# Kernel tuning notes

Measured on AMD Instinct MI355X. Metric: run time of the kernel, lower is better.

The kernel has to match this reference:

```python
import jax, jax.numpy as jnp
import numpy as np
import math

B, N, DIM, H, DH = 4, 1024, 512, 8, 64
INNER = H * DH
TEMP = 0.1
REG_LAMBDA = 0.3
LARGE_NEG = -1.0e9


def setup_inputs() -> dict:
    key = jax.random.key(0)
    ks = jax.random.split(key, 10)
    x = jax.random.normal(ks[0], (B, N, DIM), dtype=jnp.float32)
    # binary channel mask with guaranteed self-connection on the diagonal
    m = jax.random.randint(ks[1], (B, N, N), 0, 2, dtype=jnp.int32)
    eye_i = jnp.eye(N, dtype=jnp.int32)[None]
    attn_mask = jnp.maximum(m, eye_i)
    s = 0.02
    Wq = jax.random.normal(ks[2], (DIM, INNER), dtype=jnp.float32) * s
    bq = jnp.zeros((INNER,), dtype=jnp.float32)
    Wk = jax.random.normal(ks[3], (DIM, INNER), dtype=jnp.float32) * s
    bk = jnp.zeros((INNER,), dtype=jnp.float32)
    Wv = jax.random.normal(ks[4], (DIM, INNER), dtype=jnp.float32) * s
    bv = jnp.zeros((INNER,), dtype=jnp.float32)
    Wo = jax.random.normal(ks[5], (INNER, DIM), dtype=jnpp_dummy()) * s if False else jax.random.normal(ks[5], (INNER, DIM), dtype=jnp.float32) * s
    bo = jnp.zeros((DIM,), dtype=jnp.float32)
    return {"x": x, "attn_mask": attn_mask, "Wq": Wq, "bq": bq, "Wk": Wk,
            "bk": bk, "Wv": Wv, "bv": bv, "Wo": Wo, "bo": bo}


def jnp_dummy():
    return jnp.float32


def _split_heads(t):
    # [b, n, h*d] -> [b, h, n, d]
    return t.reshape(t.shape[0], t.shape[1], H, DH).transpose(0, 2, 1, 3)


def _dynamical_contrastive_loss(scores, attn_mask_f, norm_matrix):
    # cosine similarity matrix (scores / |q||k|)
    cos = scores / norm_matrix
    e = jnp.exp(cos / TEMP)                                   # [b,h,n,n]
    pos = (e * attn_mask_f[:, None]).sum(-1)                  # [b,h,n]
    allsum = e.sum(-1)                                        # [b,h,n]
    clustering = -jnp.log(pos / allsum)
    eye = jnp.eye(N, dtype=attn_mask_f.dtype)
    regular = jnp.abs(attn_mask_f - eye[None]).sum((-2, -1)) / (N * (N - 1))
    return clustering.mean() + REG_LAMBDA * regular.mean()


def reference(x, attn_mask, Wq, bq, Wk, bk, Wv, bv, Wo, bo):
    q = _split_heads(x @ Wq + bq)  # [b,h,n,d]
    k = _split_heads(x @ Wk + bk)
    v = _split_heads(x @ Wv + bv)
    scale = 1.0 / math.sqrt(DH)

    scores = jnp.einsum('bhid,bhjd->bhij', q, k)
    q_norm = jnp.linalg.norm(q, axis=-1, keepdims=True)       # [b,h,n,1]
    k_norm = jnp.linalg.norm(k, axis=-1, keepdims=True)
    norm_matrix = q_norm * jnp.swapaxes(k_norm, -1, -2)       # [b,h,n,n]

    am = attn_mask.astype(scores.dtype)[:, None]              # [b,1,n,n]
    masked_scores = scores * am + (1.0 - am) * LARGE_NEG
    # faithful replication of the all-blocked-row special case
    # (-1e9 is finite so this is a no-op unless scores contain -inf)
    row_all_blocked = jnp.all(jnp.isneginf(masked_scores), axis=-1, keepdims=True)
    masked_scores = jnp.where(row_all_blocked, jnp.zeros_like(masked_scores), masked_scores)

    dcl = _dynamical_contrastive_loss(scores, attn_mask.astype(scores.dtype), norm_matrix)

    attn = jax.nn.softmax(masked_scores * scale, axis=-1)
    out = jnp.einsum('bhij,bhjd->bhid', attn, v)
    out = out.transpose(0, 2, 1, 3).reshape(x.shape[0], x.shape[1], INNER)
    # dropout is identity in eval mode
    return out @ Wo + bo, attn, dcl
```

## Files before the change

### kernel.cpp

```cpp
#include <hip/hip_runtime.h>
#include <hip/hip_bf16.h>
#include <math.h>

#define BB 4
#define NTOK 1024
#define DIMD 512
#define HH 8
#define DH 64
#define INNER 512
#define BH (BB*HH)
#define ROWS (BB*NTOK)
#define SCALE 0.125f
#define INV_TEMP 10.0f

typedef __bf16 bf16_t;
using bf16x4 = __attribute__((ext_vector_type(4))) __bf16;
using bf16x8 = __attribute__((ext_vector_type(8))) __bf16;
using f32x4  = __attribute__((ext_vector_type(4))) float;

__device__ __forceinline__ int swz(int row, int e) { return e ^ ((row & 7) << 3); }

template<int TM, int TN, int MT, int NT>
__device__ __forceinline__ void gemm_core(
    const bf16_t* __restrict__ A, int ldA,
    const bf16_t* __restrict__ B, int ldB, int K,
    bf16_t* As, bf16_t* Bs, f32x4 (&acc)[MT][NT])
{
    const int t = threadIdx.x;
    const int w = t >> 6, l = t & 63;
    constexpr int WGN = TN / (NT * 16);
    const int wm = w / WGN, wn = w % WGN;
    const int lrow = l & 15, lk = (l >> 4) * 8;

    for (int k0 = 0; k0 < K; k0 += 32) {
        #pragma unroll
        for (int it = 0; it < TM / 64; ++it) {
            int r = (t >> 2) + it * 64;
            *(uint4*)&As[r * 32 + (t & 3) * 8] =
                *(const uint4*)&A[(size_t)r * ldA + k0 + (t & 3) * 8];
        }
        #pragma unroll
        for (int it = 0; it < TN / 64; ++it) {
            int r = (t >> 2) + it * 64;
            *(uint4*)&Bs[r * 32 + (t & 3) * 8] =
                *(const uint4*)&B[(size_t)r * ldB + k0 + (t & 3) * 8];
        }
        __syncthreads();
        bf16x8 af[MT], bf[NT];
        #pragma unroll
        for (int mt = 0; mt < MT; ++mt)
            af[mt] = *(const bf16x8*)&As[(wm * MT * 16 + mt * 16 + lrow) * 32 + lk];
        #pragma unroll
        for (int nt = 0; nt < NT; ++nt)
            bf[nt] = *(const bf16x8*)&Bs[(wn * NT * 16 + nt * 16 + lrow) * 32 + lk];
        #pragma unroll
        for (int mt = 0; mt < MT; ++mt)
            #pragma unroll
            for (int nt = 0; nt < NT; ++nt)
                acc[mt][nt] = __builtin_amdgcn_mfma_f32_16x16x32_bf16(
                    af[mt], bf[nt], acc[mt][nt], 0, 0, 0);
        __syncthreads();
    }
}

__global__ __launch_bounds__(256) void convert_x(
    const float* __restrict__ x, bf16_t* __restrict__ xb)
{
    int idx = blockIdx.x * 256 + threadIdx.x;
    float4 v = ((const float4*)x)[idx];
    bf16x4 o = { (bf16_t)v.x, (bf16_t)v.y, (bf16_t)v.z, (bf16_t)v.w };
    ((bf16x4*)xb)[idx] = o;
}

__global__ __launch_bounds__(256) void mask_pack(
    const int* __restrict__ mask, unsigned int* __restrict__ mp)
{
    const int rr = blockIdx.x, b = blockIdx.y, c = threadIdx.x;
    const int* mb = mask + ((size_t)(b * NTOK + rr * 4)) * NTOK;
    #pragma unroll
    for (int u = 0; u < 4; ++u) {
        int col = u * 256 + c;
        unsigned int o = (unsigned)mb[col]
                       | ((unsigned)mb[NTOK + col] << 8)
                       | ((unsigned)mb[2 * NTOK + col] << 16)
                       | ((unsigned)mb[3 * NTOK + col] << 24);
        mp[((size_t)b * 256 + rr) * NTOK + col] = o;
    }
}

__global__ __launch_bounds__(256) void transpose_w(
    const float* __restrict__ Wq, const float* __restrict__ Wk,
    const float* __restrict__ Wv, const float* __restrict__ Wo,
    bf16_t* __restrict__ wt)
{
    __shared__ float tile[32][33];
    const int z = blockIdx.z;
    const float* src = (z == 0) ? Wq : (z == 1) ? Wk : (z == 2) ? Wv : Wo;
    bf16_t* dst = wt + (size_t)z * DIMD * INNER;
    const int t = threadIdx.x, tx = t & 31, ty = t >> 5;
    const int rBase = blockIdx.y * 32, cBase = blockIdx.x * 32;
    #pragma unroll
    for (int i = 0; i < 4; ++i)
        tile[ty + i * 8][tx] = src[(size_t)(rBase + ty + i * 8) * INNER + cBase + tx];
    __syncthreads();
    #pragma unroll
    for (int i = 0; i < 4; ++i)
        dst[(size_t)(cBase + ty + i * 8) * DIMD + rBase + tx] = (bf16_t)tile[tx][ty + i * 8];
}

__global__ __launch_bounds__(256) void qkv_gemm(
    const bf16_t* __restrict__ xb, const bf16_t* __restrict__ wt,
    const float* __restrict__ bq, const float* __restrict__ bk,
    const float* __restrict__ bv,
    bf16_t* __restrict__ qb, bf16_t* __restrict__ kb, bf16_t* __restrict__ vt)
{
    __shared__ __align__(16) bf16_t As[128 * 32];
    __shared__ __align__(16) bf16_t Bs[128 * 32];
    const int z = blockIdx.z;
    const bf16_t* Bp = wt + (size_t)z * DIMD * INNER;
    const float* bias = (z == 0) ? bq : (z == 1) ? bk : bv;
    const int rowBase = blockIdx.y * 128, colBase = blockIdx.x * 128;

    f32x4 acc[4][4] = {};
    gemm_core<128, 128, 4, 4>(xb + (size_t)rowBase * DIMD, DIMD,
                              Bp + (size_t)colBase * DIMD, DIMD, DIMD,
                              As, Bs, acc);

    const int l = threadIdx.x & 63, w = threadIdx.x >> 6;
    const int wm = w >> 1, wn = w & 1;
    #pragma unroll
    for (int mt = 0; mt < 4; ++mt)
        #pragma unroll
        for (int nt = 0; nt < 4; ++nt)
            #pragma unroll
            for (int r = 0; r < 4; ++r) {
                int grow = rowBase + wm * 64 + mt * 16 + (l >> 4) * 4 + r;
                int gcol = colBase + wn * 64 + nt * 16 + (l & 15);
                float val = acc[mt][nt][r] + bias[gcol];
                int b = grow >> 10, n = grow & 1023, h = gcol >> 6, d = gcol & 63;
                if (z == 0)
                    qb[(((size_t)b * HH + h) * NTOK + n) * DH + d] = (bf16_t)val;
                else if (z == 1)
                    kb[(((size_t)b * HH + h) * NTOK + n) * DH + d] = (bf16_t)val;
                else
                    vt[(((size_t)b * HH + h) * DH + d) * NTOK + n] = (bf16_t)val;
            }
}

__global__ __launch_bounds__(256) void norm_kernel(
    const bf16_t* __restrict__ qb, const bf16_t* __restrict__ kb,
    float* __restrict__ iqn, float* __restrict__ ikn)
{
    const int row = blockIdx.x * 4 + (threadIdx.x >> 6);
    const int d = threadIdx.x & 63;
    const bf16_t* src = blockIdx.y ? kb : qb;
    float* dst = blockIdx.y ? ikn : iqn;
    float v = (float)src[(size_t)row * DH + d];
    float s = v * v;
    #pragma unroll
    for (int off = 32; off; off >>= 1) s += __shfl_down(s, off);
    if (d == 0) dst[row] = 1.0f / sqrtf(s);
}

__global__ __launch_bounds__(256) void stats_gemm(
    const bf16_t* __restrict__ qb, const bf16_t* __restrict__ kb,
    const unsigned int* __restrict__ mp,
    const float* __restrict__ iqn, const float* __restrict__ ikn,
    float* __restrict__ invE, float* __restrict__ cl, float* __restrict__ rg)
{
    __shared__ __align__(16) bf16_t Ks[128 * 64];
    const int bh = blockIdx.y;
    const int b = bh >> 3, h = bh & 7;
    const int rowBase = blockIdx.x * 64;
    const bf16_t* Q = qb + (size_t)bh * NTOK * DH;
    const bf16_t* K = kb + (size_t)bh * NTOK * DH;
    const float* iknr = ikn + (size_t)bh * NTOK;
    const int t = threadIdx.x, w = t >> 6, l = t & 63;
    const int l15 = l & 15, q = l >> 4;

    bf16x8 af[2];
    {
        const bf16_t* qrow = Q + (size_t)(rowBase + w * 16 + l15) * DH + q * 8;
        af[0] = *(const bf16x8*)(qrow);
        af[1] = *(const bf16x8*)(qrow + 32);
    }
    const int tok = rowBase + w * 16 + q * 4;
    float iqn4[4];
    #pragma unroll
    for (int r = 0; r < 4; ++r)
        iqn4[r] = iqn[(size_t)bh * NTOK + tok + r];

    float alls[4] = {}, pos[4] = {}, esum[4] = {}, regf[4] = {};
    const unsigned int* mrow = mp + ((size_t)b * 256 + (tok >> 2)) * NTOK;

    for (int ct = 0; ct < 8; ++ct) {
        const int col0 = ct * 128;
        #pragma unroll
        for (int u = 0; u < 4; ++u) {
            int idx = u * 256 + t;
            int kr = idx >> 3, ce = (idx & 7) * 8;
            *(uint4*)&Ks[kr * 64 + swz(kr, ce)] =
                *(const uint4*)&K[(size_t)(col0 + kr) * DH + ce];
        }
        __syncthreads();
        f32x4 sacc[8] = {};
        #pragma unroll
        for (int ks = 0; ks < 2; ++ks) {
            int koff = ks * 32 + q * 8;
            #pragma unroll
            for (int nt = 0; nt < 8; ++nt) {
                int kr = nt * 16 + l15;
                bf16x8 bfk = *(const bf16x8*)&Ks[kr * 64 + swz(kr, koff)];
                sacc[nt] = __builtin_amdgcn_mfma_f32_16x16x32_bf16(af[ks], bfk, sacc[nt], 0, 0, 0);
            }
        }
        #pragma unroll
        for (int nt = 0; nt < 8; ++nt) {
            int c = col0 + nt * 16 + l15;
            float ik = iknr[c];
            unsigned int mm = mrow[c];
            #pragma unroll
            for (int r = 0; r < 4; ++r) {
                float s = sacc[nt][r];
                float mbit = (float)((mm >> (8 * r)) & 1u);
                float e1 = __expf(s * iqn4[r] * ik * INV_TEMP);
                float e2 = __expf(s * SCALE);
                alls[r] += e1;
                pos[r]  += e1 * mbit;
                esum[r] += e2 * mbit;
                regf[r] += mbit;
            }
        }
        __syncthreads();
    }
    #pragma unroll
    for (int r = 0; r < 4; ++r) {
        #pragma unroll
        for (int off = 8; off; off >>= 1) {
            alls[r] += __shfl_xor(alls[r], off);
            pos[r]  += __shfl_xor(pos[r], off);
            esum[r] += __shfl_xor(esum[r], off);
            regf[r] += __shfl_xor(regf[r], off);
        }
    }
    if (l15 == 0) {
        #pragma unroll
        for (int r = 0; r < 4; ++r) {
            int rowG = bh * NTOK + tok + r;
            invE[rowG] = 1.0f / esum[r];
            cl[rowG] = logf(alls[r]) - logf(pos[r]);
            if (h == 0) rg[b * NTOK + tok + r] = regf[r] - 1.0f;
        }
    }
}

__global__ __launch_bounds__(256) void pav_gemm(
    const bf16_t* __restrict__ qb, const bf16_t* __restrict__ kb,
    const bf16_t* __restrict__ vt, const unsigned int* __restrict__ mp,
    const float* __restrict__ invE,
    float* __restrict__ attnf, bf16_t* __restrict__ ctxb)
{
    __shared__ __align__(16) bf16_t Ks[128 * 64];
    __shared__ __align__(16) bf16_t Vs[64 * 128];
    __shared__ __align__(16) bf16_t Ps[4 * 16 * 128];
    const int bh = blockIdx.y;
    const int b = bh >> 3, h = bh & 7;
    const int rowBase = blockIdx.x * 64;
    const bf16_t* Q = qb + (size_t)bh * NTOK * DH;
    const bf16_t* K = kb + (size_t)bh * NTOK * DH;
    const bf16_t* V = vt + (size_t)bh * DH * NTOK;
    const int t = threadIdx.x, w = t >> 6, l = t & 63;
    const int l15 = l & 15, q = l >> 4;
    bf16_t* Pw = Ps + w * (16 * 128);

    bf16x8 af[2];
    {
        const bf16_t* qrow = Q + (size_t)(rowBase + w * 16 + l15) * DH + q * 8;
        af[0] = *(const bf16x8*)(qrow);
        af[1] = *(const bf16x8*)(qrow + 32);
    }
    const int tok = rowBase + w * 16 + q * 4;
    float inv4[4];
    #pragma unroll
    for (int r = 0; r < 4; ++r)
        inv4[r] = invE[(size_t)bh * NTOK + tok + r];
    const unsigned int* mrow = mp + ((size_t)b * 256 + (tok >> 2)) * NTOK;
    float* prow = attnf + ((size_t)bh * NTOK + tok) * NTOK;

    f32x4 cacc[4] = {};

    for (int ct = 0; ct < 8; ++ct) {
        const int col0 = ct * 128;
        #pragma unroll
        for (int u = 0; u < 4; ++u) {
            int idx = u * 256 + t;
            int kr = idx >> 3, ce = (idx & 7) * 8;
            *(uint4*)&Ks[kr * 64 + swz(kr, ce)] =
                *(const uint4*)&K[(size_t)(col0 + kr) * DH + ce];
        }
        #pragma unroll
        for (int u = 0; u < 4; ++u) {
            int idx = u * 256 + t;
            int d = idx >> 4, ce = (idx & 15) * 8;
            *(uint4*)&Vs[d * 128 + swz(d, ce)] =
                *(const uint4*)&V[(size_t)d * NTOK + col0 + ce];
        }
        __syncthreads();
        f32x4 sacc[8] = {};
        #pragma unroll
        for (int ks = 0; ks < 2; ++ks) {
            int koff = ks * 32 + q * 8;
            #pragma unroll
            for (int nt = 0; nt < 8; ++nt) {
                int kr = nt * 16 + l15;
                bf16x8 bfk = *(const bf16x8*)&Ks[kr * 64 + swz(kr, koff)];
                sacc[nt] = __builtin_amdgcn_mfma_f32_16x16x32_bf16(af[ks], bfk, sacc[nt], 0, 0, 0);
            }
        }
        #pragma unroll
        for (int nt = 0; nt < 8; ++nt) {
            int c = nt * 16 + l15;
            unsigned int mm = mrow[col0 + c];
            #pragma unroll
            for (int r = 0; r < 4; ++r) {
                float p = ((mm >> (8 * r)) & 1u)
                        ? __expf(sacc[nt][r] * SCALE) * inv4[r] : 0.0f;
                prow[(size_t)r * NTOK + col0 + c] = p;
                int pr = q * 4 + r;
                Pw[pr * 128 + swz(pr, c)] = (bf16_t)p;
            }
        }
        #pragma unroll
        for (int ks = 0; ks < 4; ++ks) {
            int koff = ks * 32 + q * 8;
            bf16x8 afp = *(const bf16x8*)&Pw[l15 * 128 + swz(l15, koff)];
            #pragma unroll
            for (int nt = 0; nt < 4; ++nt) {
                int d = nt * 16 + l15;
                bf16x8 bfv = *(const bf16x8*)&Vs[d * 128 + swz(d, koff)];
                cacc[nt] = __builtin_amdgcn_mfma_f32_16x16x32_bf16(afp, bfv, cacc[nt], 0, 0, 0);
            }
        }
        __syncthreads();
    }
    #pragma unroll
    for (int nt = 0; nt < 4; ++nt)
        #pragma unroll
        for (int r = 0; r < 4; ++r) {
            int n = tok + r;
            int d = nt * 16 + l15;
            ctxb[((size_t)b * NTOK + n) * INNER + h * DH + d] = (bf16_t)cacc[nt][r];
        }
}

__device__ __forceinline__ float block_sum(float v, float* sh)
{
    #pragma unroll
    for (int off = 32; off; off >>= 1) v += __shfl_down(v, off);
    __syncthreads();
    if ((threadIdx.x & 63) == 0) sh[threadIdx.x >> 6] = v;
    __syncthreads();
    return sh[0] + sh[1] + sh[2] + sh[3];
}

__global__ __launch_bounds__(256) void finalize_kernel(
    const float* __restrict__ cl, const float* __restrict__ rg,
    float* __restrict__ dcl)
{
    __shared__ float sh[4];
    float s1 = 0.f, s2 = 0.f;
    for (int idx = threadIdx.x; idx < BH * NTOK; idx += 256) s1 += cl[idx];
    for (int idx = threadIdx.x; idx < BB * NTOK; idx += 256) s2 += rg[idx];
    s1 = block_sum(s1, sh);
    s2 = block_sum(s2, sh);
    if (threadIdx.x == 0) {
        dcl[0] = s1 * (1.0f / (float)(BB * HH * NTOK))
               + 0.3f * s2 * (1.0f / ((float)NTOK * (float)(NTOK - 1) * (float)BB));
    }
}

__global__ __launch_bounds__(256) void out_gemm(
    const bf16_t* __restrict__ ctxb, const bf16_t* __restrict__ wt,
    const float* __restrict__ bo, float* __restrict__ outp)
{
    __shared__ __align__(16) bf16_t As[128 * 32];
    __shared__ __align__(16) bf16_t Bs[128 * 32];
    const int rowBase = blockIdx.y * 128, colBase = blockIdx.x * 128;
    const bf16_t* Wot = wt + (size_t)3 * DIMD * INNER;

    f32x4 acc[4][4] = {};
    gemm_core<128, 128, 4, 4>(ctxb + (size_t)rowBase * INNER, INNER,
                              Wot + (size_t)colBase * INNER, INNER, INNER,
                              As, Bs, acc);

    const int l = threadIdx.x & 63, w = threadIdx.x >> 6;
    const int wm = w >> 1, wn = w & 1;
    #pragma unroll
    for (int mt = 0; mt < 4; ++mt)
        #pragma unroll
        for (int nt = 0; nt < 4; ++nt)
            #pragma unroll
            for (int r = 0; r < 4; ++r) {
                int grow = rowBase + wm * 64 + mt * 16 + (l >> 4) * 4 + r;
                int gcol = colBase + wn * 64 + nt * 16 + (l & 15);
                outp[(size_t)grow * DIMD + gcol] = acc[mt][nt][r] + bo[gcol];
            }
}

extern "C" void kernel_launch(void* const* d_in, const int* in_sizes, int n_in,
                              void* d_out, int out_size, void* d_ws, size_t ws_size,
                              hipStream_t stream)
{
    const float* x  = (const float*)d_in[0];
    const int* mask = (const int*)d_in[1];
    const float* Wq = (const float*)d_in[2];
    const float* bq = (const float*)d_in[3];
    const float* Wk = (const float*)d_in[4];
    const float* bk = (const float*)d_in[5];
    const float* Wv = (const float*)d_in[6];
    const float* bv = (const float*)d_in[7];
    const float* Wo = (const float*)d_in[8];
    const float* bo = (const float*)d_in[9];

    float* out   = (float*)d_out;
    float* attnf = out + (size_t)ROWS * DIMD;
    float* dcl   = attnf + (size_t)BH * NTOK * NTOK;

    char* wsb = (char*)d_ws;
    bf16_t* xb    = (bf16_t*)wsb;
    bf16_t* wt    = xb + (size_t)ROWS * DIMD;
    bf16_t* qb    = wt + (size_t)4 * DIMD * INNER;
    bf16_t* kb    = qb + (size_t)BH * NTOK * DH;
    bf16_t* vt    = kb + (size_t)BH * NTOK * DH;
    bf16_t* ctxb  = vt + (size_t)BH * NTOK * DH;
    float*  iqn   = (float*)(ctxb + (size_t)ROWS * INNER);
    float*  ikn   = iqn + BH * NTOK;
    float*  invE  = ikn + BH * NTOK;
    float*  cl    = invE + BH * NTOK;
    float*  rg    = cl + BH * NTOK;
    unsigned int* mpk = (unsigned int*)(rg + BB * NTOK);

    dim3 blk(256);
    convert_x<<<dim3(ROWS * DIMD / 1024), blk, 0, stream>>>(x, xb);
    transpose_w<<<dim3(16, 16, 4), blk, 0, stream>>>(Wq, Wk, Wv, Wo, wt);
    mask_pack<<<dim3(256, BB), blk, 0, stream>>>(mask, mpk);
    qkv_gemm<<<dim3(4, 32, 3), blk, 0, stream>>>(xb, wt, bq, bk, bv, qb, kb, vt);
    norm_kernel<<<dim3(BH * NTOK / 4, 2), blk, 0, stream>>>(qb, kb, iqn, ikn);
    stats_gemm<<<dim3(16, 32), blk, 0, stream>>>(qb, kb, mpk, iqn, ikn, invE, cl, rg);
    pav_gemm<<<dim3(16, 32), blk, 0, stream>>>(qb, kb, vt, mpk, invE, attnf, ctxb);
    out_gemm<<<dim3(4, 32), blk, 0, stream>>>(ctxb, wt, bo, out);
    finalize_kernel<<<1, blk, 0, stream>>>(cl, rg, dcl);
}
```

Baseline: 300.0 us.

## Fuse prep, norm, stats/PV and finalize kernels; use direct global-to-LDS loads

Measured after the change: 289.8 us. 3.4% less time.

```diff
diff --git a/kernel.cpp b/kernel.cpp
--- a/kernel.cpp
+++ b/kernel.cpp
@@ -20,6 +20,13 @@
 
 __device__ __forceinline__ int swz(int row, int e) { return e ^ ((row & 7) << 3); }
 
+__device__ __forceinline__ void gload_lds16(const bf16_t* g, bf16_t* l)
+{
+    __builtin_amdgcn_global_load_lds(
+        (const __attribute__((address_space(1))) void*)g,
+        (__attribute__((address_space(3))) void*)l, 16, 0, 0);
+}
+
 template<int TM, int TN, int MT, int NT>
 __device__ __forceinline__ void gemm_core(
     const bf16_t* __restrict__ A, int ldA,
@@ -36,14 +43,14 @@
         #pragma unroll
         for (int it = 0; it < TM / 64; ++it) {
             int r = (t >> 2) + it * 64;
-            *(uint4*)&As[r * 32 + (t & 3) * 8] =
-                *(const uint4*)&A[(size_t)r * ldA + k0 + (t & 3) * 8];
+            gload_lds16(&A[(size_t)r * ldA + k0 + (t & 3) * 8],
+                        As + ((size_t)it * 256 + w * 64) * 8);
         }
         #pragma unroll
         for (int it = 0; it < TN / 64; ++it) {
             int r = (t >> 2) + it * 64;
-            *(uint4*)&Bs[r * 32 + (t & 3) * 8] =
-                *(const uint4*)&B[(size_t)r * ldB + k0 + (t & 3) * 8];
+            gload_lds16(&B[(size_t)r * ldB + k0 + (t & 3) * 8],
+                        Bs + ((size_t)it * 256 + w * 64) * 8);
         }
         __syncthreads();
         bf16x8 af[MT], bf[NT];
@@ -63,56 +70,57 @@
     }
 }
 
-__global__ __launch_bounds__(256) void convert_x(
-    const float* __restrict__ x, bf16_t* __restrict__ xb)
-{
-    int idx = blockIdx.x * 256 + threadIdx.x;
-    float4 v = ((const float4*)x)[idx];
-    bf16x4 o = { (bf16_t)v.x, (bf16_t)v.y, (bf16_t)v.z, (bf16_t)v.w };
-    ((bf16x4*)xb)[idx] = o;
-}
-
-__global__ __launch_bounds__(256) void mask_pack(
-    const int* __restrict__ mask, unsigned int* __restrict__ mp)
-{
-    const int rr = blockIdx.x, b = blockIdx.y, c = threadIdx.x;
-    const int* mb = mask + ((size_t)(b * NTOK + rr * 4)) * NTOK;
-    #pragma unroll
-    for (int u = 0; u < 4; ++u) {
-        int col = u * 256 + c;
-        unsigned int o = (unsigned)mb[col]
-                       | ((unsigned)mb[NTOK + col] << 8)
-                       | ((unsigned)mb[2 * NTOK + col] << 16)
-                       | ((unsigned)mb[3 * NTOK + col] << 24);
-        mp[((size_t)b * 256 + rr) * NTOK + col] = o;
-    }
-}
-
-__global__ __launch_bounds__(256) void transpose_w(
+__global__ __launch_bounds__(256) void prep_kernel(
+    const float* __restrict__ x,
     const float* __restrict__ Wq, const float* __restrict__ Wk,
     const float* __restrict__ Wv, const float* __restrict__ Wo,
-    bf16_t* __restrict__ wt)
+    const int* __restrict__ mask,
+    bf16_t* __restrict__ xb, bf16_t* __restrict__ wt,
+    unsigned int* __restrict__ mp)
 {
     __shared__ float tile[32][33];
-    const int z = blockIdx.z;
-    const float* src = (z == 0) ? Wq : (z == 1) ? Wk : (z == 2) ? Wv : Wo;
-    bf16_t* dst = wt + (size_t)z * DIMD * INNER;
-    const int t = threadIdx.x, tx = t & 31, ty = t >> 5;
-    const int rBase = blockIdx.y * 32, cBase = blockIdx.x * 32;
-    #pragma unroll
-    for (int i = 0; i < 4; ++i)
-        tile[ty + i * 8][tx] = src[(size_t)(rBase + ty + i * 8) * INNER + cBase + tx];
-    __syncthreads();
-    #pragma unroll
-    for (int i = 0; i < 4; ++i)
-        dst[(size_t)(cBase + ty + i * 8) * DIMD + rBase + tx] = (bf16_t)tile[tx][ty + i * 8];
+    const int bid = blockIdx.x, t = threadIdx.x;
+    if (bid < 2048) {
+        int idx = bid * 256 + t;
+        float4 v = ((const float4*)x)[idx];
+        bf16x4 o = { (bf16_t)v.x, (bf16_t)v.y, (bf16_t)v.z, (bf16_t)v.w };
+        ((bf16x4*)xb)[idx] = o;
+    } else if (bid < 3072) {
+        int f = bid - 2048;
+        int bx = f & 15, by = (f >> 4) & 15, z = f >> 8;
+        const float* src = (z == 0) ? Wq : (z == 1) ? Wk : (z == 2) ? Wv : Wo;
+        bf16_t* dst = wt + (size_t)z * DIMD * INNER;
+        const int tx = t & 31, ty = t >> 5;
+        const int rBase = by * 32, cBase = bx * 32;
+        #pragma unroll
+        for (int i = 0; i < 4; ++i)
+            tile[ty + i * 8][tx] = src[(size_t)(rBase + ty + i * 8) * INNER + cBase + tx];
+        __syncthreads();
+        #pragma unroll
+        for (int i = 0; i < 4; ++i)
+            dst[(size_t)(cBase + ty + i * 8) * DIMD + rBase + tx] = (bf16_t)tile[tx][ty + i * 8];
+    } else {
+        int f = bid - 3072;
+        int rr = f & 255, b = f >> 8;
+        const int* mb = mask + ((size_t)(b * NTOK + rr * 4)) * NTOK;
+        #pragma unroll
+        for (int u = 0; u < 4; ++u) {
+            int col = u * 256 + t;
+            unsigned int o = (unsigned)mb[col]
+                           | ((unsigned)mb[NTOK + col] << 8)
+                           | ((unsigned)mb[2 * NTOK + col] << 16)
+                           | ((unsigned)mb[3 * NTOK + col] << 24);
+            mp[((size_t)b * 256 + rr) * NTOK + col] = o;
+        }
+    }
 }
 
 __global__ __launch_bounds__(256) void qkv_gemm(
     const bf16_t* __restrict__ xb, const bf16_t* __restrict__ wt,
     const float* __restrict__ bq, const float* __restrict__ bk,
     const float* __restrict__ bv,
-    bf16_t* __restrict__ qb, bf16_t* __restrict__ kb, bf16_t* __restrict__ vt)
+    bf16_t* __restrict__ qb, bf16_t* __restrict__ kb, bf16_t* __restrict__ vt,
+    float* __restrict__ iqn, float* __restrict__ ikn)
 {
     __shared__ __align__(16) bf16_t As[128 * 32];
     __shared__ __align__(16) bf16_t Bs[128 * 32];
@@ -128,6 +136,7 @@
 
     const int l = threadIdx.x & 63, w = threadIdx.x >> 6;
     const int wm = w >> 1, wn = w & 1;
+    float nsum[4][4] = {};
     #pragma unroll
     for (int mt = 0; mt < 4; ++mt)
         #pragma unroll
@@ -137,46 +146,78 @@
                 int grow = rowBase + wm * 64 + mt * 16 + (l >> 4) * 4 + r;
                 int gcol = colBase + wn * 64 + nt * 16 + (l & 15);
                 float val = acc[mt][nt][r] + bias[gcol];
+                bf16_t vb16 = (bf16_t)val;
                 int b = grow >> 10, n = grow & 1023, h = gcol >> 6, d = gcol & 63;
                 if (z == 0)
-                    qb[(((size_t)b * HH + h) * NTOK + n) * DH + d] = (bf16_t)val;
+                    qb[(((size_t)b * HH + h) * NTOK + n) * DH + d] = vb16;
                 else if (z == 1)
-                    kb[(((size_t)b * HH + h) * NTOK + n) * DH + d] = (bf16_t)val;
+                    kb[(((size_t)b * HH + h) * NTOK + n) * DH + d] = vb16;
                 else
-                    vt[(((size_t)b * HH + h) * DH + d) * NTOK + n] = (bf16_t)val;
-            }
-}
-
-__global__ __launch_bounds__(256) void norm_kernel(
+                    vt[(((size_t)b * HH + h) * DH + d) * NTOK + n] = vb16;
+                if (z < 2) { float vb = (float)vb16; nsum[mt][r] += vb * vb; }
+            }
+    if (z < 2) {
+        float* dst = (z == 0) ? iqn : ikn;
+        const int h = (colBase >> 6) + wn;
+        #pragma unroll
+        for (int mt = 0; mt < 4; ++mt)
+            #pragma unroll
+            for (int r = 0; r < 4; ++r) {
+                float s = nsum[mt][r];
+                s += __shfl_xor(s, 8); s += __shfl_xor(s, 4);
+                s += __shfl_xor(s, 2); s += __shfl_xor(s, 1);
+                if ((l & 15) == 0) {
+                    int grow = rowBase + wm * 64 + mt * 16 + (l >> 4) * 4 + r;
+                    int b = grow >> 10, n = grow & 1023;
+                    dst[((size_t)b * HH + h) * NTOK + n] = 1.0f / sqrtf(s);
+                }
+            }
+    }
+}
+
+__device__ __forceinline__ void stage_k(const bf16_t* K, int col0, bf16_t* Ks, int t)
+{
+    const int w = t >> 6, l = t & 63;
+    #pragma unroll
+    for (int u = 0; u < 4; ++u) {
+        int g = u * 256 + w * 64 + l;
+        int kr = g >> 3, ep = (g & 7) * 8;
+        gload_lds16(K + (size_t)(col0 + kr) * DH + (ep ^ ((kr & 7) << 3)),
+                    Ks + ((size_t)u * 256 + w * 64) * 8);
+    }
+}
+__device__ __forceinline__ void stage_v(const bf16_t* V, int col0, bf16_t* Vs, int t)
+{
+    const int w = t >> 6, l = t & 63;
+    #pragma unroll
+    for (int u = 0; u < 4; ++u) {
+        int g = u * 256 + w * 64 + l;
+        int d = g >> 4, ep = (g & 15) * 8;
+        gload_lds16(V + (size_t)d * NTOK + col0 + (ep ^ ((d & 7) << 3)),
+                    Vs + ((size_t)u * 256 + w * 64) * 8);
+    }
+}
+
+__global__ __launch_bounds__(256) void attn_fused(
     const bf16_t* __restrict__ qb, const bf16_t* __restrict__ kb,
-    float* __restrict__ iqn, float* __restrict__ ikn)
-{
-    const int row = blockIdx.x * 4 + (threadIdx.x >> 6);
-    const int d = threadIdx.x & 63;
-    const bf16_t* src = blockIdx.y ? kb : qb;
-    float* dst = blockIdx.y ? ikn : iqn;
-    float v = (float)src[(size_t)row * DH + d];
-    float s = v * v;
-    #pragma unroll
-    for (int off = 32; off; off >>= 1) s += __shfl_down(s, off);
-    if (d == 0) dst[row] = 1.0f / sqrtf(s);
-}
-
-__global__ __launch_bounds__(256) void stats_gemm(
-    const bf16_t* __restrict__ qb, const bf16_t* __restrict__ kb,
-    const unsigned int* __restrict__ mp,
+    const bf16_t* __restrict__ vt, const unsigned int* __restrict__ mp,
     const float* __restrict__ iqn, const float* __restrict__ ikn,
-    float* __restrict__ invE, float* __restrict__ cl, float* __restrict__ rg)
+    float* __restrict__ attnf, bf16_t* __restrict__ ctxb,
+    float* __restrict__ cl, float* __restrict__ rg)
 {
     __shared__ __align__(16) bf16_t Ks[128 * 64];
+    __shared__ __align__(16) bf16_t Vs[64 * 128];
+    __shared__ __align__(16) bf16_t Ps[4 * 16 * 128];
     const int bh = blockIdx.y;
     const int b = bh >> 3, h = bh & 7;
     const int rowBase = blockIdx.x * 64;
     const bf16_t* Q = qb + (size_t)bh * NTOK * DH;
     const bf16_t* K = kb + (size_t)bh * NTOK * DH;
+    const bf16_t* V = vt + (size_t)bh * DH * NTOK;
     const float* iknr = ikn + (size_t)bh * NTOK;
     const int t = threadIdx.x, w = t >> 6, l = t & 63;
     const int l15 = l & 15, q = l >> 4;
+    bf16_t* Pw = Ps + w * (16 * 128);
 
     bf16x8 af[2];
     {
@@ -189,19 +230,13 @@
     #pragma unroll
     for (int r = 0; r < 4; ++r)
         iqn4[r] = iqn[(size_t)bh * NTOK + tok + r];
+    const unsigned int* mrow = mp + ((size_t)b * 256 + (tok >> 2)) * NTOK;
 
     float alls[4] = {}, pos[4] = {}, esum[4] = {}, regf[4] = {};
-    const unsigned int* mrow = mp + ((size_t)b * 256 + (tok >> 2)) * NTOK;
 
     for (int ct = 0; ct < 8; ++ct) {
         const int col0 = ct * 128;
-        #pragma unroll
-        for (int u = 0; u < 4; ++u) {
-            int idx = u * 256 + t;
-            int kr = idx >> 3, ce = (idx & 7) * 8;
-            *(uint4*)&Ks[kr * 64 + swz(kr, ce)] =
-                *(const uint4*)&K[(size_t)(col0 + kr) * DH + ce];
-        }
+        stage_k(K, col0, Ks, t);
         __syncthreads();
         f32x4 sacc[8] = {};
         #pragma unroll
@@ -233,6 +268,7 @@
         }
         __syncthreads();
     }
+    float inv4[4];
     #pragma unroll
     for (int r = 0; r < 4; ++r) {
         #pragma unroll
@@ -242,69 +278,23 @@
             esum[r] += __shfl_xor(esum[r], off);
             regf[r] += __shfl_xor(regf[r], off);
         }
+        inv4[r] = 1.0f / esum[r];
     }
     if (l15 == 0) {
         #pragma unroll
         for (int r = 0; r < 4; ++r) {
             int rowG = bh * NTOK + tok + r;
-            invE[rowG] = 1.0f / esum[r];
             cl[rowG] = logf(alls[r]) - logf(pos[r]);
             if (h == 0) rg[b * NTOK + tok + r] = regf[r] - 1.0f;
         }
     }
-}
-
-__global__ __launch_bounds__(256) void pav_gemm(
-    const bf16_t* __restrict__ qb, const bf16_t* __restrict__ kb,
-    const bf16_t* __restrict__ vt, const unsigned int* __restrict__ mp,
-    const float* __restrict__ invE,
-    float* __restrict__ attnf, bf16_t* __restrict__ ctxb)
-{
-    __shared__ __align__(16) bf16_t Ks[128 * 64];
-    __shared__ __align__(16) bf16_t Vs[64 * 128];
-    __shared__ __align__(16) bf16_t Ps[4 * 16 * 128];
-    const int bh = blockIdx.y;
-    const int b = bh >> 3, h = bh & 7;
-    const int rowBase = blockIdx.x * 64;
-    const bf16_t* Q = qb + (size_t)bh * NTOK * DH;
-    const bf16_t* K = kb + (size_t)bh * NTOK * DH;
-    const bf16_t* V = vt + (size_t)bh * DH * NTOK;
-    const int t = threadIdx.x, w = t >> 6, l = t & 63;
-    const int l15 = l & 15, q = l >> 4;
-    bf16_t* Pw = Ps + w * (16 * 128);
-
-    bf16x8 af[2];
-    {
-        const bf16_t* qrow = Q + (size_t)(rowBase + w * 16 + l15) * DH + q * 8;
-        af[0] = *(const bf16x8*)(qrow);
-        af[1] = *(const bf16x8*)(qrow + 32);
-    }
-    const int tok = rowBase + w * 16 + q * 4;
-    float inv4[4];
-    #pragma unroll
-    for (int r = 0; r < 4; ++r)
-        inv4[r] = invE[(size_t)bh * NTOK + tok + r];
-    const unsigned int* mrow = mp + ((size_t)b * 256 + (tok >> 2)) * NTOK;
+
     float* prow = attnf + ((size_t)bh * NTOK + tok) * NTOK;
-
     f32x4 cacc[4] = {};
-
     for (int ct = 0; ct < 8; ++ct) {
         const int col0 = ct * 128;
-        #pragma unroll
-        for (int u = 0; u < 4; ++u) {
-            int idx = u * 256 + t;
-            int kr = idx >> 3, ce = (idx & 7) * 8;
-            *(uint4*)&Ks[kr * 64 + swz(kr, ce)] =
-                *(const uint4*)&K[(size_t)(col0 + kr) * DH + ce];
-        }
-        #pragma unroll
-        for (int u = 0; u < 4; ++u) {
-            int idx = u * 256 + t;
-            int d = idx >> 4, ce = (idx & 15) * 8;
-            *(uint4*)&Vs[d * 128 + swz(d, ce)] =
-                *(const uint4*)&V[(size_t)d * NTOK + col0 + ce];
-        }
+        stage_k(K, col0, Ks, t);
+        stage_v(V, col0, Vs, t);
         __syncthreads();
         f32x4 sacc[8] = {};
         #pragma unroll
@@ -363,28 +353,15 @@
     return sh[0] + sh[1] + sh[2] + sh[3];
 }
 
-__global__ __launch_bounds__(256) void finalize_kernel(
+__global__ __launch_bounds__(256) void out_gemm(
+    const bf16_t* __restrict__ ctxb, const bf16_t* __restrict__ wt,
+    const float* __restrict__ bo, float* __restrict__ outp,
     const float* __restrict__ cl, const float* __restrict__ rg,
     float* __restrict__ dcl)
 {
-    __shared__ float sh[4];
-    float s1 = 0.f, s2 = 0.f;
-    for (int idx = threadIdx.x; idx < BH * NTOK; idx += 256) s1 += cl[idx];
-    for (int idx = threadIdx.x; idx < BB * NTOK; idx += 256) s2 += rg[idx];
-    s1 = block_sum(s1, sh);
-    s2 = block_sum(s2, sh);
-    if (threadIdx.x == 0) {
-        dcl[0] = s1 * (1.0f / (float)(BB * HH * NTOK))
-               + 0.3f * s2 * (1.0f / ((float)NTOK * (float)(NTOK - 1) * (float)BB));
-    }
-}
-
-__global__ __launch_bounds__(256) void out_gemm(
-    const bf16_t* __restrict__ ctxb, const bf16_t* __restrict__ wt,
-    const float* __restrict__ bo, float* __restrict__ outp)
-{
     __shared__ __align__(16) bf16_t As[128 * 32];
     __shared__ __align__(16) bf16_t Bs[128 * 32];
+    __shared__ float sh4[4];
     const int rowBase = blockIdx.y * 128, colBase = blockIdx.x * 128;
     const bf16_t* Wot = wt + (size_t)3 * DIMD * INNER;
 
@@ -405,6 +382,19 @@
                 int gcol = colBase + wn * 64 + nt * 16 + (l & 15);
                 outp[(size_t)grow * DIMD + gcol] = acc[mt][nt][r] + bo[gcol];
             }
+
+    if (blockIdx.x == 0 && blockIdx.y == 0) {
+        float s1 = 0.f, s2 = 0.f;
+        for (int idx = threadIdx.x; idx < BH * NTOK; idx += 256) s1 += cl[idx];
+        for (int idx = threadIdx.x; idx < BB * NTOK; idx += 256) s2 += rg[idx];
+        __syncthreads();
+        s1 = block_sum(s1, sh4);
+        s2 = block_sum(s2, sh4);
+        if (threadIdx.x == 0) {
+            dcl[0] = s1 * (1.0f / (float)(BB * HH * NTOK))
+                   + 0.3f * s2 * (1.0f / ((float)NTOK * (float)(NTOK - 1) * (float)BB));
+        }
+    }
 }
 
 extern "C" void kernel_launch(void* const* d_in, const int* in_sizes, int n_in,
@@ -435,19 +425,13 @@
     bf16_t* ctxb  = vt + (size_t)BH * NTOK * DH;
     float*  iqn   = (float*)(ctxb + (size_t)ROWS * INNER);
     float*  ikn   = iqn + BH * NTOK;
-    float*  invE  = ikn + BH * NTOK;
-    float*  cl    = invE + BH * NTOK;
+    float*  cl    = ikn + BH * NTOK;
     float*  rg    = cl + BH * NTOK;
     unsigned int* mpk = (unsigned int*)(rg + BB * NTOK);
 
     dim3 blk(256);
-    convert_x<<<dim3(ROWS * DIMD / 1024), blk, 0, stream>>>(x, xb);
-    transpose_w<<<dim3(16, 16, 4), blk, 0, stream>>>(Wq, Wk, Wv, Wo, wt);
-    mask_pack<<<dim3(256, BB), blk, 0, stream>>>(mask, mpk);
-    qkv_gemm<<<dim3(4, 32, 3), blk, 0, stream>>>(xb, wt, bq, bk, bv, qb, kb, vt);
-    norm_kernel<<<dim3(BH * NTOK / 4, 2), blk, 0, stream>>>(qb, kb, iqn, ikn);
-    stats_gemm<<<dim3(16, 32), blk, 0, stream>>>(qb, kb, mpk, iqn, ikn, invE, cl, rg);
-    pav_gemm<<<dim3(16, 32), blk, 0, stream>>>(qb, kb, vt, mpk, invE, attnf, ctxb);
-    out_gemm<<<dim3(4, 32), blk, 0, stream>>>(ctxb, wt, bo, out);
-    finalize_kernel<<<1, blk, 0, stream>>>(cl, rg, dcl);
-}
+    prep_kernel<<<dim3(4096), blk, 0, stream>>>(x, Wq, Wk, Wv, Wo, mask, xb, wt, mpk);
+    qkv_gemm<<<dim3(4, 32, 3), blk, 0, stream>>>(xb, wt, bq, bk, bv, qb, kb, vt, iqn, ikn);
+    attn_fused<<<dim3(16, 32), blk, 0, stream>>>(qb, kb, vt, mpk, iqn, ikn, attnf, ctxb, cl, rg);
+    out_gemm<<<dim3(4, 32), blk, 0, stream>>>(ctxb, wt, bo, out, cl, rg, dcl);
+}
```
